# Kernel tuning notes

Measured on AMD Instinct MI355X. Metric: run time of the kernel, lower is better.

The kernel has to match this reference:

```python
import jax, jax.numpy as jnp
import numpy as np

# ---- problem constants (the torch module's `params` dict) ----
D = H = W = 128          # volume_shape
HS = WS = 128            # slice_shape
N_SLICES = 16
PSF = 3                  # PSF kernel is PSF^3 taps
K = PSF ** 3
RES_RATIO = 1.5          # res_s / res_r: slice pixel spacing in volume-voxel units
N_ITER = 10              # CG iterations (tol = 0.0 -> fixed trip count)
PSF_SIGMA = 0.8


def _corners(pts):
    """8-corner trilinear indices/weights with zero contribution out of bounds.
    pts: [..., 3] in (x, y, z) voxel coords. Returns (list of int32 linear idx, list of weights).
    Gather and scatter share this so A and At are exact transposes (required for CG)."""
    x, y, z = pts[..., 0], pts[..., 1], pts[..., 2]
    x0f, y0f, z0f = jnp.floor(x), jnp.floor(y), jnp.floor(z)
    fx, fy, fz = x - x0f, y - y0f, z - z0f
    x0, y0, z0 = x0f.astype(jnp.int32), y0f.astype(jnp.int32), z0f.astype(jnp.int32)
    idxs, ws = [], []
    for dz in (0, 1):
        for dy in (0, 1):
            for dx in (0, 1):
                xi, yi, zi = x0 + dx, y0 + dy, z0 + dz
                w = (fx if dx else 1.0 - fx) * (fy if dy else 1.0 - fy) * (fz if dz else 1.0 - fz)
                inb = (xi >= 0) & (xi < W) & (yi >= 0) & (yi < H) & (zi >= 0) & (zi < D)
                idxs.append(jnp.where(inb, (zi * H + yi) * W + xi, 0))
                ws.append(jnp.where(inb, w, 0.0))
    return idxs, ws


def _sample_points(transforms):
    """PSF sample points of every slice pixel mapped into volume voxel coords.
    transforms: [N, 3, 4] rigid (R | t). Returns [N, HS, WS, K, 3] in (x, y, z)."""
    u = (jnp.arange(WS, dtype=jnp.float32) - (WS - 1) / 2) * RES_RATIO
    v = (jnp.arange(HS, dtype=jnp.float32) - (HS - 1) / 2) * RES_RATIO
    base = jnp.stack(jnp.broadcast_arrays(u[None, :], v[:, None], jnp.zeros((HS, WS), jnp.float32)), -1)  # [HS,WS,3]
    ax = jnp.arange(PSF, dtype=jnp.float32) - (PSF - 1) / 2
    oz, oy, ox = jnp.meshgrid(ax, ax, ax, indexing='ij')
    offs = jnp.stack([ox.ravel(), oy.ravel(), oz.ravel()], -1)            # [K,3] voxel units
    pts = base[:, :, None, :] + offs[None, None, :, :]                     # [HS,WS,K,3] in slice frame
    R, t = transforms[:, :3, :3], transforms[:, :3, 3]
    pts = jnp.einsum('hwkc,nrc->nhwkr', pts, R) + t[:, None, None, None, :]
    center = jnp.array([(W - 1) / 2, (H - 1) / 2, (D - 1) / 2], jnp.float32)
    return pts + center


def A_op(transforms, vol, psf_flat):
    """slice_acquisition: PSF-weighted trilinear gather from volume -> slices [N,1,HS,WS]."""
    pts = _sample_points(transforms)
    flat = vol.reshape(-1)
    idxs, ws = _corners(pts)
    vals = sum(w * flat[i] for i, w in zip(idxs, ws))                      # [N,HS,WS,K]
    return jnp.einsum('nhwk,k->nhw', vals, psf_flat)[:, None]


def At_op(transforms, slices, psf_flat):
    """slice_acquisition_adjoint: PSF-weighted trilinear scatter-add of slices -> volume."""
    pts = _sample_points(transforms)
    wv = slices[:, 0, :, :, None] * psf_flat                               # [N,HS,WS,K]
    idxs, ws = _corners(pts)
    flat = jnp.zeros(D * H * W, slices.dtype)
    for i, w in zip(idxs, ws):
        flat = flat.at[i.reshape(-1)].add((w * wv).reshape(-1))
    return flat.reshape(1, 1, D, H, W)


def _dot(a, b):
    return jnp.vdot(a.reshape(-1), b.reshape(-1))


def cg_solve(AtA, b, x0, n_iter):
    r0 = b - AtA(x0)
    def body(state, _):
        x, r, p, rr = state
        Ap = AtA(p)
        alpha = rr / _dot(p, Ap)
        x = x + alpha * p
        r = r - alpha * Ap
        rr_new = _dot(r, r)
        p = r + (rr_new / rr) * p
        return (x, r, p, rr_new), None
    (x, _, _, _), _ = jax.lax.scan(body, (x0, r0, r0, _dot(r0, r0)), None, length=n_iter)
    return x


def _rigid_transforms(n, rng):
    # small random rotations (Rodrigues) + z-stacked translations, like motion-corrupted slice stacks
    ang = rng.uniform(-0.1, 0.1, (n, 3)).astype(np.float32)
    mats = []
    for a in ang:
        th = float(np.linalg.norm(a)) + 1e-8
        k = a / th
        Kx = np.array([[0, -k[2], k[1]], [k[2], 0, -k[0]], [-k[1], k[0], 0]], np.float32)
        mats.append(np.eye(3, dtype=np.float32) + np.sin(th) * Kx + (1 - np.cos(th)) * (Kx @ Kx))
    R = np.stack(mats)
    t = np.zeros((n, 3), np.float32)
    t[:, 2] = (np.arange(n) - (n - 1) / 2) * RES_RATIO
    t[:, :2] = rng.uniform(-2.0, 2.0, (n, 2)).astype(np.float32)
    return jnp.asarray(np.concatenate([R, t[:, :, None]], axis=-1))        # [n,3,4]


def setup_inputs() -> dict:
    key = jax.random.key(0)
    k1, k2 = jax.random.split(key)
    rng = np.random.default_rng(0)
    theta = _rigid_transforms(N_SLICES, rng)
    slices = jax.random.uniform(k1, (N_SLICES, 1, HS, WS), jnp.float32)
    volume = jax.random.uniform(k2, (1, 1, D, H, W), jnp.float32)
    ax = np.arange(PSF) - (PSF - 1) / 2
    zz, yy, xx = np.meshgrid(ax, ax, ax, indexing='ij')
    psf = np.exp(-(xx ** 2 + yy ** 2 + zz ** 2) / (2 * PSF_SIGMA ** 2)).astype(np.float32)
    psf /= psf.sum()
    return {"theta": theta, "slices": slices, "volume": volume, "psf": jnp.asarray(psf)}


def reference(theta, slices, volume, psf):
    psf_flat = psf.reshape(-1)
    AtA = lambda v: At_op(theta, A_op(theta, v, psf_flat), psf_flat)
    b = At_op(theta, slices, psf_flat)          # b = At(y); p is None, mu = 0
    x = cg_solve(AtA, b, volume, N_ITER)
    return jax.nn.relu(x)                       # output_relu=True
```

## Files before the change

### kernel.cpp

```cpp
#include <hip/hip_runtime.h>
#include <math.h>

constexpr int VOX = 128 * 128 * 128;
constexpr int NPIX = 16 * 128 * 128;
constexpr int NS = 16;
constexpr float RES_RATIO = 1.5f;
constexpr int CSTR = 128;
constexpr int TNX = 19, TNY = 19, TNZ = 10;
constexpr int ZSL = 5;


__global__ __launch_bounds__(512) void prep_kernel(
    const float* __restrict__ theta, const float* __restrict__ psf,
    float* __restrict__ cst, int* __restrict__ zb)
{
    int tid = threadIdx.x;
    int n = tid >> 5, j = tid & 31;
    if (n < NS) {
        const float* T = theta + n * 12;
        float* C = cst + n * CSTR;
        if (j < 12) C[j] = T[j];
        if (j == 12) {
            float r00=T[0], r01=T[1], r02=T[2],  t0=T[3];
            float r10=T[4], r11=T[5], r12=T[6],  t1=T[7];
            float r20=T[8], r21=T[9], r22=T[10], t2=T[11];
            float tc0 = t0 + 63.5f, tc1 = t1 + 63.5f, tc2 = t2 + 63.5f;
            C[12]=tc0; C[13]=tc1; C[14]=tc2;
            float C2 = fabsf(r02)+fabsf(r12)+fabsf(r22);
            C[15] = fabsf(r00)+fabsf(r10)+fabsf(r20);
            C[16] = fabsf(r01)+fabsf(r11)+fabsf(r21);
            C[17] = C2;
            C[18] = fabsf(r00)+fabsf(r01)+fabsf(r02);
            C[19] = fabsf(r10)+fabsf(r11)+fabsf(r12);
            C[20] = fabsf(r20)+fabsf(r21)+fabsf(r22);
            float mx = fmaxf(tc0, 127.0f - tc0);
            float my = fmaxf(tc1, 127.0f - tc1);
            float marg = 1.05f + C2 + fabsf(r02)*mx + fabsf(r12)*my;
            float inv = 1.0f / fabsf(r22);
            C[21] = tc2 - marg * inv;
            C[22] = tc2 + marg * inv;
            C[105] = 1.0f + C2 + 0.01f;
            C[106] = 1.0f / r22;
            C[107] = -(r20 * tc2);
            C[108] = -(r21 * tc2);
            C[109] = -(r22 * tc2);
        }
        if (j < 27) {
            float ox = (float)(j % 3) - 1.0f;
            float oy = (float)((j / 3) % 3) - 1.0f;
            float oz = (float)(j / 9) - 1.0f;
            C[24 + 3*j + 0] = T[0]*ox + T[1]*oy + T[2]*oz;
            C[24 + 3*j + 1] = T[4]*ox + T[5]*oy + T[6]*oz;
            C[24 + 3*j + 2] = T[8]*ox + T[9]*oy + T[10]*oz;
        }
    }
    __syncthreads();
    if (tid == 0) {
        float zmin = 1e30f, zmax = -1e30f;
        for (int s = 0; s < NS; ++s) {
            zmin = fminf(zmin, cst[s * CSTR + 21]);
            zmax = fmaxf(zmax, cst[s * CSTR + 22]);
        }
        zb[0] = max(0, (int)floorf(zmin));
        zb[1] = min(127, (int)ceilf(zmax));
        float* G = cst + NS * CSTR;
        float c = psf[13];
        float ic2 = 1.0f / (c * c);
        G[0]=psf[12]; G[1]=psf[13]; G[2]=psf[14];
        G[3]=psf[10]; G[4]=psf[13]; G[5]=psf[16];
        G[6]=psf[4]*ic2; G[7]=psf[13]*ic2; G[8]=psf[22]*ic2;
    }
}

__device__ __forceinline__ void block_reduce_spread(double s, double* slots)
{
    #pragma unroll
    for (int off = 32; off > 0; off >>= 1)
        s += __shfl_down(s, off, 64);
    __shared__ double ls[4];
    if ((threadIdx.x & 63) == 0) ls[threadIdx.x >> 6] = s;
    __syncthreads();
    if (threadIdx.x == 0)
        atomicAdd(&slots[(blockIdx.x & 63) * 32], ls[0] + ls[1] + ls[2] + ls[3]);
}

__device__ __forceinline__ void block_reduce3(
    double s0, double s1, double s2, double* a0, double* a1, double* a2)
{
    #pragma unroll
    for (int off = 32; off > 0; off >>= 1) {
        s0 += __shfl_down(s0, off, 64);
        s1 += __shfl_down(s1, off, 64);
        s2 += __shfl_down(s2, off, 64);
    }
    __shared__ double ls3[12];
    int wid = threadIdx.x >> 6;
    if ((threadIdx.x & 63) == 0) {
        ls3[wid*3+0] = s0; ls3[wid*3+1] = s1; ls3[wid*3+2] = s2;
    }
    __syncthreads();
    if (threadIdx.x == 0) {
        int sl = (blockIdx.x & 63) * 32;
        atomicAdd(&a0[sl], ls3[0]+ls3[3]+ls3[6]+ls3[9]);
        atomicAdd(&a1[sl], ls3[1]+ls3[4]+ls3[7]+ls3[10]);
        atomicAdd(&a2[sl], ls3[2]+ls3[5]+ls3[8]+ls3[11]);
    }
}

__global__ __launch_bounds__(64, 4) void a_kernel(
    const float* __restrict__ cst, const float* __restrict__ vol,
    const float* __restrict__ psf, float* __restrict__ out,
    const float* __restrict__ subsrc,
    double* __restrict__ z1, double* __restrict__ z2, double* __restrict__ z3)
{
    int tid = threadIdx.x;
    if (blockIdx.x == 0) {
        for (int i = tid; i < 2048; i += 64) {
            if (z1) z1[i] = 0.0;
            if (z2) z2[i] = 0.0;
            if (z3) z3[i] = 0.0;
        }
    }

    int b = blockIdx.x;
    int n = b >> 8;
    int pb = b & 255;
    int w0 = (pb & 15) << 3, h0 = (pb >> 4) << 3;
    int w = w0 + (tid & 7), h = h0 + (tid >> 3);
    int oidx = (n << 14) + (h << 7) + w;
    float base = subsrc ? subsrc[oidx] : 0.0f;
    float sgn = subsrc ? -1.0f : 1.0f;

    const float* C = cst + n * CSTR;
    float r00=C[0], r01=C[1];
    float r10=C[4], r11=C[5];
    float r20=C[8], r21=C[9];

    float uc = (w0 + 3.5f - 63.5f) * RES_RATIO;
    float vc = (h0 + 3.5f - 63.5f) * RES_RATIO;
    const float du = 5.25f, dv = 5.25f;
    float cx = r00*uc + r01*vc + C[12];
    float cy = r10*uc + r11*vc + C[13];
    float cz = r20*uc + r21*vc + C[14];
    float hx = fabsf(r00)*du + fabsf(r01)*dv + C[18];
    float hy = fabsf(r10)*du + fabsf(r11)*dv + C[19];
    float hz = fabsf(r20)*du + fabsf(r21)*dv + C[20];
    int tx0 = (int)floorf(cx - hx);
    int ty0 = (int)floorf(cy - hy);
    int tz0 = (int)floorf(cz - hz);

    if (tx0 >= 128 || tx0 + TNX <= 0 || ty0 >= 128 || ty0 + TNY <= 0 ||
        tz0 >= 128 || tz0 + TNZ <= 0) {
        out[oidx] = base;
        return;
    }

    __shared__ float tile[TNZ * TNY * TNX];
    for (int i = tid; i < TNZ * TNY * TNX; i += 64) {
        int xx = i % TNX; int rem = i / TNX;
        int yy = rem % TNY; int zz = rem / TNY;
        int gx = tx0 + xx, gy = ty0 + yy, gz = tz0 + zz;
        bool ok = ((unsigned)gx < 128u) & ((unsigned)gy < 128u) & ((unsigned)gz < 128u);
        int off = ok ? ((gz << 14) + (gy << 7) + gx) : 0;
        float v = vol[off];
        tile[i] = ok ? v : 0.0f;
    }
    __syncthreads();

    float u = (w - 63.5f) * RES_RATIO;
    float v = (h - 63.5f) * RES_RATIO;
    float px = fmaf(r00, u, fmaf(r01, v, C[12])) - (float)tx0;
    float py = fmaf(r10, u, fmaf(r11, v, C[13])) - (float)ty0;
    float pz = fmaf(r20, u, fmaf(r21, v, C[14])) - (float)tz0;

    const float* O = C + 24;
    float acc = 0.0f;
    for (int k = 0; k < 27; ++k) {
        float sx = px + O[3*k+0];
        float sy = py + O[3*k+1];
        float sz = pz + O[3*k+2];
        int x0 = (int)sx, y0 = (int)sy, z0 = (int)sz;
        float fx = sx - (float)x0, fy = sy - (float)y0, fz = sz - (float)z0;
        const float* tp = tile + (z0 * TNY + y0) * TNX + x0;
        float c000 = tp[0],             c001 = tp[1];
        float c010 = tp[TNX],           c011 = tp[TNX+1];
        float c100 = tp[TNY*TNX],       c101 = tp[TNY*TNX+1];
        float c110 = tp[TNY*TNX+TNX],   c111 = tp[TNY*TNX+TNX+1];
        float c00 = fmaf(fx, c001 - c000, c000);
        float c01 = fmaf(fx, c011 - c010, c010);
        float c10 = fmaf(fx, c101 - c100, c100);
        float c11 = fmaf(fx, c111 - c110, c110);
        float c0  = fmaf(fy, c01 - c00, c00);
        float c1  = fmaf(fy, c11 - c10, c10);
        acc = fmaf(psf[k], fmaf(fz, c1 - c0, c0), acc);
    }
    out[oidx] = fmaf(sgn, acc, base);
}

#define ATS_CL(B_) fmaxf(1.0f - fabsf(B_), 0.0f)
#define ATS_PT(cAi, cBi, cCi, Xai, Yai, Zai, SEL, fyj, mvj, ACC) { \
    float sf_  = SEL(cAi, cBi, cCi); \
    float svf_ = sf_ * fyj; \
    float Bx_ = fmaf(r01, mvj, Xai); \
    float By_ = fmaf(r11, mvj, Yai); \
    float Bz_ = fmaf(r21, mvj, Zai); \
    float w0_ = ATS_CL(Bx_ - r02) * ATS_CL(By_ - r12) * ATS_CL(Bz_ - r22); \
    float w1_ = ATS_CL(Bx_) * ATS_CL(By_) * ATS_CL(Bz_); \
    float w2_ = ATS_CL(Bx_ + r02) * ATS_CL(By_ + r12) * ATS_CL(Bz_ + r22); \
    float t_  = fmaf(w0_, pfz0, fmaf(w1_, pfz1, w2_ * pfz2)); \
    ACC = fmaf(t_, svf_, ACC); }
#define ATS_ROW(SEL, fyj, mvj) \
    ATS_PT(cA0,cB0,cC0, Xa0,Ya0,Za0, SEL, fyj, mvj, acc0) \
    ATS_PT(cA1,cB1,cC1, Xa1,Ya1,Za1, SEL, fyj, mvj, acc1) \
    ATS_PT(cA2,cB2,cC2, Xa2,Ya2,Za2, SEL, fyj, mvj, acc0) \
    ATS_PT(cA3,cB3,cC3, Xa3,Ya3,Za3, SEL, fyj, mvj, acc1) \
    ATS_PT(cA4,cB4,cC4, Xa4,Ya4,Za4, SEL, fyj, mvj, acc0)
#define SEL_J0(a,b,c) (mj1 ? (b) : (a))
#define SEL_J1(a,b,c) (mj1 ? (a) : (b))
#define SEL_J2(a,b,c) (mj1 ? (b) : (mj2 ? (c) : (a)))
#define SEL_J3(a,b,c) (mj1 ? (c) : (b))
#define SEL_J4(a,b,c) (mj1 ? (b) : (c))

__global__ __launch_bounds__(256, 4) void at_scatter_kernel(
    const float* __restrict__ cst, const float* __restrict__ sl,
    float* __restrict__ outvol)
{
    int id = blockIdx.x * 256 + threadIdx.x;
    int x = id & 127, y = (id >> 7) & 127;
    int n = (id >> 14) & 15, zi = id >> 18;
    const float* C = cst + n * CSTR;
    float r00=C[0], r01=C[1], r02=C[2];
    float r10=C[4], r11=C[5], r12=C[6];
    float r20=C[8], r21=C[9], r22=C[10];
    float tc2 = C[14];
    float C0=C[15], C1=C[16];

    float gx = (float)x - C[12];
    float gy = (float)y - C[13];

    float az = r02*gx + r12*gy + C[109];
    float lim = C[105];
    float inv22 = C[106];
    int z0 = (int)ceilf((-lim - az) * inv22);
    int z1v = (int)floorf(( lim - az) * inv22);
    z0 = max(z0, 0); z1v = min(z1v, 127);
    int z = z0 + zi;
    if (z > z1v) return;

    float ax = r00*gx + r10*gy + C[107];
    float ay = r01*gx + r11*gy + C[108];

    float fzv = (float)z;
    float gpx = fmaf(r20, fzv, ax);
    float gpy = fmaf(r21, fzv, ay);
    float gz  = fzv - tc2;
    int m2 = (int)floorf(2.0f*(gpx + 95.25f - C0)) + 601;
    int n2 = (int)floorf(2.0f*(gpy + 95.25f - C1)) + 601;
    int wb0 = m2 / 3;
    int hb0 = n2 / 3;
    int ki0 = m2 - wb0 * 3;
    int kj0 = n2 - hb0 * 3;

    const float* slice_n = sl + (n << 14);
    float s[3][3];
    #pragma unroll
    for (int aa = 0; aa < 3; ++aa) {
        int hv = hb0 - 200 + aa;
        bool hok = ((unsigned)hv < 128u);
        #pragma unroll
        for (int cc = 0; cc < 3; ++cc) {
            int wv = wb0 - 200 + cc;
            bool ok = hok & ((unsigned)wv < 128u);
            int off = ok ? ((hv << 7) + wv) : 0;
            float vs = slice_n[off];
            s[aa][cc] = ok ? vs : 0.0f;
        }
    }

    const float* G = cst + NS * CSTR;
    float pfx0=G[0], pfx1=G[1], pfx2=G[2];
    float pfy0=G[3], pfy1=G[4], pfy2=G[5];
    float pfz0=G[6], pfz1=G[7], pfz2=G[8];

    int yx = (y << 7) + x;

    bool mi1 = (ki0 == 1), mi2 = (ki0 == 2);
    bool mj1 = (kj0 == 1), mj2 = (kj0 == 2);

    float fxA = mi1 ? pfx0 : (mi2 ? pfx2 : pfx1);
    float fxB = mi1 ? pfx2 : (mi2 ? pfx1 : pfx0);
    float fxC = mi1 ? pfx1 : (mi2 ? pfx0 : pfx2);

    float fyA = mj1 ? pfy0 : (mj2 ? pfy2 : pfy1);
    float fyB = mj1 ? pfy2 : (mj2 ? pfy1 : pfy0);
    float fyC = mj1 ? pfy1 : (mj2 ? pfy0 : pfy2);

    float cA0 = (mi1 ? s[0][1] : s[0][0]) * fxA;
    float cB0 = (mi1 ? s[1][1] : s[1][0]) * fxA;
    float cC0 = (mi1 ? s[2][1] : s[2][0]) * fxA;
    float cA1 = (mi1 ? s[0][0] : s[0][1]) * fxB;
    float cB1 = (mi1 ? s[1][0] : s[1][1]) * fxB;
    float cC1 = (mi1 ? s[2][0] : s[2][1]) * fxB;
    float cA2 = (mi1 ? s[0][1] : (mi2 ? s[0][2] : s[0][0])) * fxC;
    float cB2 = (mi1 ? s[1][1] : (mi2 ? s[1][2] : s[1][0])) * fxC;
    float cC2 = (mi1 ? s[2][1] : (mi2 ? s[2][2] : s[2][0])) * fxC;
    float cA3 = (mi1 ? s[0][2] : s[0][1]) * fxA;
    float cB3 = (mi1 ? s[1][2] : s[1][1]) * fxA;
    float cC3 = (mi1 ? s[2][2] : s[2][1]) * fxA;
    float cA4 = (mi1 ? s[0][1] : s[0][2]) * fxB;
    float cB4 = (mi1 ? s[1][1] : s[1][2]) * fxB;
    float cC4 = (mi1 ? s[2][1] : s[2][2]) * fxB;

    float mu0_ = 0.5f * (float)(m2 - 600) - 95.25f;
    float mu1_ = 0.5f * (float)(m2 - 599) - 95.25f;
    float mu2_ = 0.5f * (float)(m2 - 598) - 95.25f;
    float mu3_ = 0.5f * (float)(m2 - 597) - 95.25f;
    float mu4_ = 0.5f * (float)(m2 - 596) - 95.25f;
    float Xa0 = fmaf(r00, mu0_, -gx), Ya0 = fmaf(r10, mu0_, -gy), Za0 = fmaf(r20, mu0_, -gz);
    float Xa1 = fmaf(r00, mu1_, -gx), Ya1 = fmaf(r10, mu1_, -gy), Za1 = fmaf(r20, mu1_, -gz);
    float Xa2 = fmaf(r00, mu2_, -gx), Ya2 = fmaf(r10, mu2_, -gy), Za2 = fmaf(r20, mu2_, -gz);
    float Xa3 = fmaf(r00, mu3_, -gx), Ya3 = fmaf(r10, mu3_, -gy), Za3 = fmaf(r20, mu3_, -gz);
    float Xa4 = fmaf(r00, mu4_, -gx), Ya4 = fmaf(r10, mu4_, -gy), Za4 = fmaf(r20, mu4_, -gz);

    asm volatile("" ::
        "v"(cA0),"v"(cA1),"v"(cA2),"v"(cA3),"v"(cA4),
        "v"(cB0),"v"(cB1),"v"(cB2),"v"(cB3),"v"(cB4),
        "v"(cC0),"v"(cC1),"v"(cC2),"v"(cC3),"v"(cC4),
        "v"(Xa0),"v"(Xa1),"v"(Xa2),"v"(Xa3),"v"(Xa4),
        "v"(Ya0),"v"(Ya1),"v"(Ya2),"v"(Ya3),"v"(Ya4),
        "v"(Za0),"v"(Za1),"v"(Za2),"v"(Za3),"v"(Za4),
        "v"(fyA),"v"(fyB),"v"(fyC));

    float mv0_ = 0.5f * (float)(n2 - 600) - 95.25f;
    float mv1_ = 0.5f * (float)(n2 - 599) - 95.25f;
    float mv2_ = 0.5f * (float)(n2 - 598) - 95.25f;
    float mv3_ = 0.5f * (float)(n2 - 597) - 95.25f;
    float mv4_ = 0.5f * (float)(n2 - 596) - 95.25f;

    float acc0 = 0.0f, acc1 = 0.0f;
    ATS_ROW(SEL_J0, fyA, mv0_)
    ATS_ROW(SEL_J1, fyB, mv1_)
    ATS_ROW(SEL_J2, fyC, mv2_)
    ATS_ROW(SEL_J3, fyA, mv3_)
    ATS_ROW(SEL_J4, fyB, mv4_)

    atomicAdd(&outvol[(z << 14) + yx], acc0 + acc1);
}

__global__ __launch_bounds__(256) void initpr_kernel(
    const float* __restrict__ r, float* __restrict__ p, float* __restrict__ Ap,
    double* __restrict__ rr_slots, const int* __restrict__ zb)
{
    int z = blockIdx.x >> 6;
    if (z < zb[0] || z > zb[1]) return;
    int i = blockIdx.x * 256 + threadIdx.x;
    float rv = r[i];
    p[i] = rv;
    Ap[i] = 0.0f;
    block_reduce_spread((double)rv * (double)rv, rr_slots);
}

__global__ __launch_bounds__(256) void dots_kernel(
    const float* __restrict__ Ap, const float* __restrict__ p,
    const float* __restrict__ r,
    double* __restrict__ s_pap, double* __restrict__ s_rap,
    double* __restrict__ s_apap, const int* __restrict__ zb)
{
    int z = blockIdx.x >> 6;
    if (z < zb[0] || z > zb[1]) return;
    int i = blockIdx.x * 256 + threadIdx.x;
    double a = (double)Ap[i];
    block_reduce3(a * (double)p[i], a * (double)r[i], a * a,
                  s_pap, s_rap, s_apap);
}

__global__ __launch_bounds__(256) void update_kernel(
    float* __restrict__ x, float* __restrict__ r, float* __restrict__ p,
    float* __restrict__ Ap,
    const double* __restrict__ rr_src, int rr_is_slots,
    const double* __restrict__ paps, const double* __restrict__ raps,
    const double* __restrict__ apaps, double* __restrict__ rr_out,
    const int* __restrict__ zb, float* __restrict__ outp)
{
    __shared__ float sh_ab[2];
    int tid = threadIdx.x;
    if (tid < 64) {
        double v0 = rr_is_slots ? rr_src[tid * 32] : 0.0;
        double v1 = paps[tid * 32];
        double v2 = raps[tid * 32];
        double v3 = apaps[tid * 32];
        #pragma unroll
        for (int off = 32; off > 0; off >>= 1) {
            v0 += __shfl_down(v0, off, 64);
            v1 += __shfl_down(v1, off, 64);
            v2 += __shfl_down(v2, off, 64);
            v3 += __shfl_down(v3, off, 64);
        }
        if (tid == 0) {
            double rr_old = rr_is_slots ? v0 : rr_src[0];
            double alpha = rr_old / v1;
            double rr_new = rr_old - 2.0 * alpha * v2 + alpha * alpha * v3;
            if (blockIdx.x == 0) rr_out[0] = rr_new;
            sh_ab[0] = (float)alpha;
            sh_ab[1] = (float)(rr_new / rr_old);
        }
    }
    __syncthreads();
    float af = sh_ab[0], bf = sh_ab[1];

    int z = blockIdx.x >> 6;
    int i = blockIdx.x * 256 + tid;
    bool inslab = (z >= zb[0]) & (z <= zb[1]);
    if (!inslab) {
        if (outp) outp[i] = fmaxf(x[i], 0.0f);
        return;
    }
    float xv = fmaf(af, p[i], x[i]);
    x[i] = xv;
    float apv = Ap[i];
    Ap[i] = 0.0f;
    float rvv = fmaf(-af, apv, r[i]);
    r[i] = rvv;
    p[i] = fmaf(bf, p[i], rvv);
    if (outp) outp[i] = fmaxf(xv, 0.0f);
}

extern "C" void kernel_launch(void* const* d_in, const int* in_sizes, int n_in,
                              void* d_out, int out_size, void* d_ws, size_t ws_size,
                              hipStream_t stream) {
    const float* theta  = (const float*)d_in[0];
    const float* slices = (const float*)d_in[1];
    const float* volume = (const float*)d_in[2];
    const float* psf    = (const float*)d_in[3];
    float* out = (float*)d_out;

    char* ws = (char*)d_ws;
    float* x  = (float*)ws;
    float* r  = x  + VOX;
    float* p  = r  + VOX;
    float* Ap = p  + VOX;
    float* sl = Ap + VOX;
    double* sc = (double*)(sl + NPIX);
    double* rrs0  = sc;
    double* paps  = sc + 2048;
    double* raps  = sc + 4096;
    double* apaps = sc + 6144;
    double* rr_sc = sc + 8192;
    float* cst = (float*)(sc + 8208);
    int* zb = (int*)(cst + NS * CSTR + 16);

    const int gapix = NPIX / 64;
    const int gvox = VOX / 256;
    const int gsc  = NPIX * ZSL / 256;

    prep_kernel<<<1, 512, 0, stream>>>(theta, psf, cst, zb);

    hipMemcpyAsync(x, volume, VOX * sizeof(float), hipMemcpyDeviceToDevice, stream);
    hipMemsetAsync(r, 0, 2 * VOX * sizeof(float), stream);

    a_kernel<<<gapix, 64, 0, stream>>>(cst, x, psf, sl, slices, rrs0, nullptr, nullptr);
    at_scatter_kernel<<<gsc, 256, 0, stream>>>(cst, sl, r);
    initpr_kernel<<<gvox, 256, 0, stream>>>(r, p, Ap, rrs0, zb);

    for (int it = 0; it < 10; ++it) {
        a_kernel<<<gapix, 64, 0, stream>>>(cst, p, psf, sl, nullptr, paps, raps, apaps);
        at_scatter_kernel<<<gsc, 256, 0, stream>>>(cst, sl, Ap);
        dots_kernel<<<gvox, 256, 0, stream>>>(Ap, p, r, paps, raps, apaps, zb);

        const double* rr_src = (it == 0) ? rrs0 : &rr_sc[it];
        update_kernel<<<gvox, 256, 0, stream>>>(
            x, r, p, Ap, rr_src, (it == 0) ? 1 : 0,
            paps, raps, apaps, &rr_sc[it + 1], zb, (it == 9) ? out : nullptr);
    }
}
```

Baseline: 869.1 us.

## Fuse CG dot products and update into one persistent grid-synced kernel

Merges the dots and update kernels into a single 1024-block grid-stride kernel. Blocks post partial dot products with atomics, and block 0 waits on an atomic counter, computes alpha and beta, then releases the other blocks through a flag. This removes one launch per CG iteration and a second pass over the volume's blocks, at the cost of a software grid barrier that assumes all 1024 blocks are co-resident. The change also steps the a_kernel tile-load indices incrementally instead of using div/mod, and simplifies the PSF-factor selects.

```diff
diff --git a/kernel.cpp b/kernel.cpp
--- a/kernel.cpp
+++ b/kernel.cpp
@@ -84,29 +84,6 @@
         atomicAdd(&slots[(blockIdx.x & 63) * 32], ls[0] + ls[1] + ls[2] + ls[3]);
 }
 
-__device__ __forceinline__ void block_reduce3(
-    double s0, double s1, double s2, double* a0, double* a1, double* a2)
-{
-    #pragma unroll
-    for (int off = 32; off > 0; off >>= 1) {
-        s0 += __shfl_down(s0, off, 64);
-        s1 += __shfl_down(s1, off, 64);
-        s2 += __shfl_down(s2, off, 64);
-    }
-    __shared__ double ls3[12];
-    int wid = threadIdx.x >> 6;
-    if ((threadIdx.x & 63) == 0) {
-        ls3[wid*3+0] = s0; ls3[wid*3+1] = s1; ls3[wid*3+2] = s2;
-    }
-    __syncthreads();
-    if (threadIdx.x == 0) {
-        int sl = (blockIdx.x & 63) * 32;
-        atomicAdd(&a0[sl], ls3[0]+ls3[3]+ls3[6]+ls3[9]);
-        atomicAdd(&a1[sl], ls3[1]+ls3[4]+ls3[7]+ls3[10]);
-        atomicAdd(&a2[sl], ls3[2]+ls3[5]+ls3[8]+ls3[11]);
-    }
-}
-
 __global__ __launch_bounds__(64, 4) void a_kernel(
     const float* __restrict__ cst, const float* __restrict__ vol,
     const float* __restrict__ psf, float* __restrict__ out,
@@ -156,14 +133,20 @@
     }
 
     __shared__ float tile[TNZ * TNY * TNX];
-    for (int i = tid; i < TNZ * TNY * TNX; i += 64) {
-        int xx = i % TNX; int rem = i / TNX;
-        int yy = rem % TNY; int zz = rem / TNY;
-        int gx = tx0 + xx, gy = ty0 + yy, gz = tz0 + zz;
-        bool ok = ((unsigned)gx < 128u) & ((unsigned)gy < 128u) & ((unsigned)gz < 128u);
-        int off = ok ? ((gz << 14) + (gy << 7) + gx) : 0;
-        float v = vol[off];
-        tile[i] = ok ? v : 0.0f;
+    {
+        int gx = tx0 + tid % TNX;
+        int gy = ty0 + tid / TNX;
+        int gz = tz0;
+        const int gxe = tx0 + TNX, gye = ty0 + TNY;
+        for (int i = tid; i < TNZ * TNY * TNX; i += 64) {
+            bool ok = ((unsigned)gx < 128u) & ((unsigned)gy < 128u) & ((unsigned)gz < 128u);
+            int off = ok ? ((gz << 14) + (gy << 7) + gx) : 0;
+            float v = vol[off];
+            tile[i] = ok ? v : 0.0f;
+            gx += 7; gy += 3;
+            if (gx >= gxe) { gx -= TNX; gy += 1; }
+            if (gy >= gye) { gy -= TNY; gz += 1; }
+        }
     }
     __syncthreads();
 
@@ -278,22 +261,22 @@
     }
 
     const float* G = cst + NS * CSTR;
-    float pfx0=G[0], pfx1=G[1], pfx2=G[2];
-    float pfy0=G[3], pfy1=G[4], pfy2=G[5];
+    float pfx0=G[0], pfx1=G[1];
+    float pfy0=G[3], pfy1=G[4];
     float pfz0=G[6], pfz1=G[7], pfz2=G[8];
 
     int yx = (y << 7) + x;
 
-    bool mi1 = (ki0 == 1), mi2 = (ki0 == 2);
-    bool mj1 = (kj0 == 1), mj2 = (kj0 == 2);
-
-    float fxA = mi1 ? pfx0 : (mi2 ? pfx2 : pfx1);
-    float fxB = mi1 ? pfx2 : (mi2 ? pfx1 : pfx0);
-    float fxC = mi1 ? pfx1 : (mi2 ? pfx0 : pfx2);
-
-    float fyA = mj1 ? pfy0 : (mj2 ? pfy2 : pfy1);
-    float fyB = mj1 ? pfy2 : (mj2 ? pfy1 : pfy0);
-    float fyC = mj1 ? pfy1 : (mj2 ? pfy0 : pfy2);
+    bool mi0 = (ki0 == 0), mi1 = (ki0 == 1), mi2 = (ki0 == 2);
+    bool mj0 = (kj0 == 0), mj1 = (kj0 == 1), mj2 = (kj0 == 2);
+
+    float fxA = mi0 ? pfx1 : pfx0;
+    float fxB = mi2 ? pfx1 : pfx0;
+    float fxC = mi1 ? pfx1 : pfx0;
+
+    float fyA = mj0 ? pfy1 : pfy0;
+    float fyB = mj2 ? pfy1 : pfy0;
+    float fyC = mj1 ? pfy1 : pfy0;
 
     float cA0 = (mi1 ? s[0][1] : s[0][0]) * fxA;
     float cB0 = (mi1 ? s[1][1] : s[1][0]) * fxA;
@@ -360,69 +343,122 @@
     block_reduce_spread((double)rv * (double)rv, rr_slots);
 }
 
-__global__ __launch_bounds__(256) void dots_kernel(
-    const float* __restrict__ Ap, const float* __restrict__ p,
-    const float* __restrict__ r,
-    double* __restrict__ s_pap, double* __restrict__ s_rap,
-    double* __restrict__ s_apap, const int* __restrict__ zb)
-{
-    int z = blockIdx.x >> 6;
-    if (z < zb[0] || z > zb[1]) return;
-    int i = blockIdx.x * 256 + threadIdx.x;
-    double a = (double)Ap[i];
-    block_reduce3(a * (double)p[i], a * (double)r[i], a * a,
-                  s_pap, s_rap, s_apap);
-}
-
-__global__ __launch_bounds__(256) void update_kernel(
+__global__ __launch_bounds__(256) void dots_update_kernel(
     float* __restrict__ x, float* __restrict__ r, float* __restrict__ p,
     float* __restrict__ Ap,
     const double* __restrict__ rr_src, int rr_is_slots,
-    const double* __restrict__ paps, const double* __restrict__ raps,
-    const double* __restrict__ apaps, double* __restrict__ rr_out,
+    double* __restrict__ paps, double* __restrict__ raps,
+    double* __restrict__ apaps, double* __restrict__ rr_out,
     const int* __restrict__ zb, float* __restrict__ outp)
 {
+    int tid = threadIdx.x;
+    int zlo = zb[0], zhi = zb[1];
+    int b0 = zlo << 6, b1 = (zhi + 1) << 6;
+
+    unsigned long long* ctr  = (unsigned long long*)(paps + 1);
+    unsigned long long* flag = (unsigned long long*)(paps + 2);
+    float* abf = (float*)(paps + 3);
+
+    double s0 = 0.0, s1 = 0.0, s2 = 0.0;
+    for (int vb = b0 + (int)blockIdx.x; vb < b1; vb += (int)gridDim.x) {
+        int i = vb * 256 + tid;
+        double a = (double)Ap[i];
+        s0 += a * (double)p[i];
+        s1 += a * (double)r[i];
+        s2 += a * a;
+    }
+    #pragma unroll
+    for (int off = 32; off > 0; off >>= 1) {
+        s0 += __shfl_down(s0, off, 64);
+        s1 += __shfl_down(s1, off, 64);
+        s2 += __shfl_down(s2, off, 64);
+    }
+    __shared__ double ls3[12];
     __shared__ float sh_ab[2];
-    int tid = threadIdx.x;
-    if (tid < 64) {
-        double v0 = rr_is_slots ? rr_src[tid * 32] : 0.0;
-        double v1 = paps[tid * 32];
-        double v2 = raps[tid * 32];
-        double v3 = apaps[tid * 32];
-        #pragma unroll
-        for (int off = 32; off > 0; off >>= 1) {
-            v0 += __shfl_down(v0, off, 64);
-            v1 += __shfl_down(v1, off, 64);
-            v2 += __shfl_down(v2, off, 64);
-            v3 += __shfl_down(v3, off, 64);
-        }
+    int wid = tid >> 6;
+    if ((tid & 63) == 0) {
+        ls3[wid*3+0] = s0; ls3[wid*3+1] = s1; ls3[wid*3+2] = s2;
+    }
+    __syncthreads();
+    if (tid == 0) {
+        int sl = (blockIdx.x & 63) * 32;
+        atomicAdd(&paps[sl],  ls3[0]+ls3[3]+ls3[6]+ls3[9]);
+        atomicAdd(&raps[sl],  ls3[1]+ls3[4]+ls3[7]+ls3[10]);
+        atomicAdd(&apaps[sl], ls3[2]+ls3[5]+ls3[8]+ls3[11]);
+        __threadfence();
+        __hip_atomic_fetch_add(ctr, 1ull, __ATOMIC_RELEASE,
+                               __HIP_MEMORY_SCOPE_AGENT);
+    }
+
+    if (blockIdx.x == 0) {
         if (tid == 0) {
-            double rr_old = rr_is_slots ? v0 : rr_src[0];
-            double alpha = rr_old / v1;
-            double rr_new = rr_old - 2.0 * alpha * v2 + alpha * alpha * v3;
-            if (blockIdx.x == 0) rr_out[0] = rr_new;
-            sh_ab[0] = (float)alpha;
-            sh_ab[1] = (float)(rr_new / rr_old);
-        }
-    }
-    __syncthreads();
+            while (__hip_atomic_load(ctr, __ATOMIC_ACQUIRE,
+                                     __HIP_MEMORY_SCOPE_AGENT)
+                   < (unsigned long long)gridDim.x)
+                __builtin_amdgcn_s_sleep(8);
+            __threadfence();
+        }
+        __syncthreads();
+        if (tid < 64) {
+            double v0 = rr_is_slots ? rr_src[tid * 32] : 0.0;
+            double v1 = paps[tid * 32];
+            double v2 = raps[tid * 32];
+            double v3 = apaps[tid * 32];
+            #pragma unroll
+            for (int off = 32; off > 0; off >>= 1) {
+                v0 += __shfl_down(v0, off, 64);
+                v1 += __shfl_down(v1, off, 64);
+                v2 += __shfl_down(v2, off, 64);
+                v3 += __shfl_down(v3, off, 64);
+            }
+            if (tid == 0) {
+                double rr_old = rr_is_slots ? v0 : rr_src[0];
+                double alpha = rr_old / v1;
+                double rr_new = rr_old - 2.0 * alpha * v2 + alpha * alpha * v3;
+                rr_out[0] = rr_new;
+                float af = (float)alpha;
+                float bf = (float)(rr_new / rr_old);
+                abf[0] = af; abf[1] = bf;
+                sh_ab[0] = af; sh_ab[1] = bf;
+                __threadfence();
+                __hip_atomic_store(flag, 1ull, __ATOMIC_RELEASE,
+                                   __HIP_MEMORY_SCOPE_AGENT);
+            }
+        }
+        __syncthreads();
+    } else {
+        if (tid == 0) {
+            while (__hip_atomic_load(flag, __ATOMIC_ACQUIRE,
+                                     __HIP_MEMORY_SCOPE_AGENT) == 0ull)
+                __builtin_amdgcn_s_sleep(8);
+            __threadfence();
+            sh_ab[0] = abf[0]; sh_ab[1] = abf[1];
+        }
+        __syncthreads();
+    }
     float af = sh_ab[0], bf = sh_ab[1];
 
-    int z = blockIdx.x >> 6;
-    int i = blockIdx.x * 256 + tid;
-    bool inslab = (z >= zb[0]) & (z <= zb[1]);
-    if (!inslab) {
-        if (outp) outp[i] = fmaxf(x[i], 0.0f);
-        return;
-    }
-    float xv = fmaf(af, p[i], x[i]);
-    x[i] = xv;
-    float apv = Ap[i];
-    Ap[i] = 0.0f;
-    float rvv = fmaf(-af, apv, r[i]);
-    r[i] = rvv;
-    p[i] = fmaf(bf, p[i], rvv);
-    if (outp) outp[i] = fmaxf(xv, 0.0f);
+    for (int vb = b0 + (int)blockIdx.x; vb < b1; vb += (int)gridDim.x) {
+        int i = vb * 256 + tid;
+        float xv = fmaf(af, p[i], x[i]);
+        x[i] = xv;
+        float apv = Ap[i];
+        Ap[i] = 0.0f;
+        float rvv = fmaf(-af, apv, r[i]);
+        r[i] = rvv;
+        p[i] = fmaf(bf, p[i], rvv);
+        if (outp) outp[i] = fmaxf(xv, 0.0f);
+    }
+    if (outp) {
+        for (int vb = (int)blockIdx.x; vb < b0; vb += (int)gridDim.x) {
+            int i = vb * 256 + tid;
+            outp[i] = fmaxf(x[i], 0.0f);
+        }
+        for (int vb = b1 + (int)blockIdx.x; vb < VOX / 256; vb += (int)gridDim.x) {
+            int i = vb * 256 + tid;
+            outp[i] = fmaxf(x[i], 0.0f);
+        }
+    }
 }
 
 extern "C" void kernel_launch(void* const* d_in, const int* in_sizes, int n_in,
@@ -452,6 +488,7 @@
     const int gapix = NPIX / 64;
     const int gvox = VOX / 256;
     const int gsc  = NPIX * ZSL / 256;
+    const int gdu  = 1024;
 
     prep_kernel<<<1, 512, 0, stream>>>(theta, psf, cst, zb);
 
@@ -465,10 +502,8 @@
     for (int it = 0; it < 10; ++it) {
         a_kernel<<<gapix, 64, 0, stream>>>(cst, p, psf, sl, nullptr, paps, raps, apaps);
         at_scatter_kernel<<<gsc, 256, 0, stream>>>(cst, sl, Ap);
-        dots_kernel<<<gvox, 256, 0, stream>>>(Ap, p, r, paps, raps, apaps, zb);
-
         const double* rr_src = (it == 0) ? rrs0 : &rr_sc[it];
-        update_kernel<<<gvox, 256, 0, stream>>>(
+        dots_update_kernel<<<gdu, 256, 0, stream>>>(
             x, r, p, Ap, rr_src, (it == 0) ? 1 : 0,
             paps, raps, apaps, &rr_sc[it + 1], zb, (it == 9) ? out : nullptr);
     }
```

After: 2.192 ms. +152.3%, slower.
